# Kernel tuning notes

Measured on AMD Instinct MI355X. Metric: run time of the kernel, lower is better.

The kernel has to match this reference:

```python
import jax, jax.numpy as jnp
import numpy as np

B, S, DIN, D = 16, 1024, 64, 64

def setup_inputs() -> dict:
    key = jax.random.key(0)
    kx, kq, kk, kv, kaK, kaV = jax.random.split(key, 6)
    w_scale = 1.0 / np.sqrt(DIN)
    x = jax.random.normal(kx, (B, S, DIN), dtype=jnp.float32)
    Wq = jax.random.normal(kq, (DIN, D), dtype=jnp.float32) * w_scale
    Wk = jax.random.normal(kk, (DIN, D), dtype=jnp.float32) * w_scale
    Wv = jax.random.normal(kv, (DIN, D), dtype=jnp.float32) * w_scale
    # relative-position bias tables alpha_K/alpha_V: [S, S, D]
    alpha_K = jax.random.normal(kaK, (S, S, D), dtype=jnp.float32) * 0.02
    alpha_V = jax.random.normal(kaV, (S, S, D), dtype=jnp.float32) * 0.02
    return {"x": x, "Wq": Wq, "Wk": Wk, "Wv": Wv,
            "alpha_K": alpha_K, "alpha_V": alpha_V}

def reference(x, Wq, Wk, Wv, alpha_K, alpha_V):
    # Relation-aware self-attention (Shaw et al. style), vectorized form of
    # the original per-query loop:
    #   score[b,i,j] = q[b,i] . (k[b,j] + alpha_K[i,j]) / sqrt(D)
    #   z[b,i]       = sum_j softmax_j(score)[b,i,j] * (v[b,j] + alpha_V[i,j])
    d = Wq.shape[1]
    inv_sqrt_d = 1.0 / np.sqrt(d)
    q = jnp.einsum('bsf,fd->bsd', x, Wq)
    k = jnp.einsum('bsf,fd->bsd', x, Wk)
    v = jnp.einsum('bsf,fd->bsd', x, Wv)
    scores = (jnp.einsum('bid,bjd->bij', q, k)
              + jnp.einsum('bid,ijd->bij', q, alpha_K)) * inv_sqrt_d
    attn = jax.nn.softmax(scores, axis=-1)  # [B, S, S]
    z = (jnp.einsum('bij,bjd->bid', attn, v)
         + jnp.einsum('bij,ijd->bid', attn, alpha_V))
    return z, attn
```

## Files before the change

kernel.cpp:

```cpp
#include <hip/hip_runtime.h>
#include <hip/hip_fp16.h>
#include <hip/hip_bf16.h>


typedef unsigned short u16;
typedef __attribute__((ext_vector_type(8))) short bhalf8;
typedef __attribute__((ext_vector_type(4))) float fx4;

__device__ __forceinline__ short b16(float f) {
  __hip_bfloat16 h = __float2bfloat16(f);
  return *reinterpret_cast<short*>(&h);
}

__device__ __forceinline__ bhalf8 pack8(float4 a, float4 b) {
  bhalf8 r;
  r[0] = b16(a.x); r[1] = b16(a.y); r[2] = b16(a.z); r[3] = b16(a.w);
  r[4] = b16(b.x); r[5] = b16(b.y); r[6] = b16(b.z); r[7] = b16(b.w);
  return r;
}

__global__ __launch_bounds__(256) void k_proj(
    const float* __restrict__ x, const float* __restrict__ Wq,
    const float* __restrict__ Wk, const float* __restrict__ Wv,
    u16* __restrict__ qbf, u16* __restrict__ kbf, float* __restrict__ vf)
{
  __shared__ float wl[3 * 4096];
  const int t = threadIdx.x;
  for (int c = t; c < 4096; c += 256) {
    wl[c] = Wq[c]; wl[4096 + c] = Wk[c]; wl[8192 + c] = Wv[c];
  }
  __syncthreads();
  const int row = blockIdx.x * 64 + (t >> 2);
  const int dbase = (t & 3) * 16;
  float xr[64];
  const float4* xp = (const float4*)(x + (size_t)row * 64);
#pragma unroll
  for (int c = 0; c < 16; ++c) {
    float4 v = xp[c];
    xr[4*c] = v.x; xr[4*c+1] = v.y; xr[4*c+2] = v.z; xr[4*c+3] = v.w;
  }
  float aq[16], ak[16], av[16];
#pragma unroll
  for (int m = 0; m < 16; ++m) { aq[m] = 0.f; ak[m] = 0.f; av[m] = 0.f; }
#pragma unroll
  for (int f = 0; f < 64; ++f) {
    const float xv = xr[f];
    const float* wq = wl + f * 64 + dbase;
#pragma unroll
    for (int m = 0; m < 16; ++m) {
      aq[m] = fmaf(xv, wq[m], aq[m]);
      ak[m] = fmaf(xv, wq[4096 + m], ak[m]);
      av[m] = fmaf(xv, wq[8192 + m], av[m]);
    }
  }
  union { u16 u[16]; uint4 q[2]; } pq, pk;
#pragma unroll
  for (int m = 0; m < 16; ++m) { pq.u[m] = (u16)b16(aq[m]); pk.u[m] = (u16)b16(ak[m]); }
  const size_t o = (size_t)row * 64 + dbase;
  *(uint4*)(qbf + o) = pq.q[0]; *(uint4*)(qbf + o + 8) = pq.q[1];
  *(uint4*)(kbf + o) = pk.q[0]; *(uint4*)(kbf + o + 8) = pk.q[1];
  float4* vo = (float4*)(vf + o);
  vo[0] = make_float4(av[0], av[1], av[2], av[3]);
  vo[1] = make_float4(av[4], av[5], av[6], av[7]);
  vo[2] = make_float4(av[8], av[9], av[10], av[11]);
  vo[3] = make_float4(av[12], av[13], av[14], av[15]);
}

__global__ __launch_bounds__(256) void k_qk(
    const u16* __restrict__ qbf, const u16* __restrict__ kbf, __half* __restrict__ qkw)
{
  const int t = threadIdx.x, l = t & 63, w = t >> 6;
  const int b = blockIdx.x & 15, it = blockIdx.x >> 4;
  const int lr = l & 15, lg = l >> 4;
  const int i0 = it * 64 + w * 16;
  const u16* qp = qbf + (size_t)(b * 1024 + i0 + lr) * 64 + lg * 8;
  bhalf8 a0 = *(const bhalf8*)(qp);
  bhalf8 a1 = *(const bhalf8*)(qp + 32);
  for (int jt = 0; jt < 64; ++jt) {
    const int j0 = jt * 16;
    const u16* kp = kbf + (size_t)(b * 1024 + j0 + lr) * 64 + lg * 8;
    bhalf8 b0 = *(const bhalf8*)(kp);
    bhalf8 b1 = *(const bhalf8*)(kp + 32);
    fx4 acc = {0.f, 0.f, 0.f, 0.f};
    acc = __builtin_amdgcn_mfma_f32_16x16x32_bf16(a0, b0, acc, 0, 0, 0);
    acc = __builtin_amdgcn_mfma_f32_16x16x32_bf16(a1, b1, acc, 0, 0, 0);
#pragma unroll
    for (int r = 0; r < 4; ++r) {
      const int i = i0 + lg * 4 + r;
      qkw[((size_t)i * 16 + b) * 1024 + j0 + lr] = __float2half(acc[r]);
    }
  }
}

#define SLD2 516
__global__ __launch_bounds__(256, 4) void k_core(
    const float* __restrict__ aK, const float* __restrict__ aV,
    const u16* __restrict__ qbf, const __half* __restrict__ qkw,
    float* __restrict__ attn_out, float* __restrict__ za)
{
  __shared__ float sl[16 * SLD2];
  __shared__ float stats[64];
  const int i = blockIdx.x;
  const int t = threadIdx.x, l = t & 63, w = t >> 6;
  const int lr = l & 15, lg = l >> 4;

  const u16* qp = qbf + (size_t)(lr * 1024 + i) * 64 + lg * 8;
  bhalf8 a0 = *(const bhalf8*)(qp);
  bhalf8 a1 = *(const bhalf8*)(qp + 32);

  float zc[16];
#pragma unroll
  for (int b = 0; b < 16; ++b) zc[b] = 0.f;

  for (int h = 0; h < 2; ++h) {
    const __half* qk = qkw + (size_t)i * 16384 + h * 512;
    for (int c = t; c < 1024; c += 256) {
      const int b = c >> 6;
      const int j8 = (c & 63) * 8;
      const __half2* hp = (const __half2*)(qk + (size_t)b * 1024 + j8);
      float2 f0 = __half22float2(hp[0]);
      float2 f1 = __half22float2(hp[1]);
      float2 f2 = __half22float2(hp[2]);
      float2 f3 = __half22float2(hp[3]);
      float* dst = sl + b * SLD2 + j8;
      *(float4*)(dst)     = make_float4(f0.x, f0.y, f1.x, f1.y);
      *(float4*)(dst + 4) = make_float4(f2.x, f2.y, f3.x, f3.y);
    }
    __syncthreads();

    for (int tt = 0; tt < 8; ++tt) {
      const int j0 = (w + tt * 4) * 16;
      const float* ap = aK + ((size_t)i * 1024 + h * 512 + j0 + lr) * 64 + lg * 8;
      float4 c0 = *(const float4*)(ap);
      float4 c1 = *(const float4*)(ap + 4);
      float4 c2 = *(const float4*)(ap + 32);
      float4 c3 = *(const float4*)(ap + 36);
      fx4 acc = {0.f, 0.f, 0.f, 0.f};
      acc = __builtin_amdgcn_mfma_f32_16x16x32_bf16(a0, pack8(c0, c1), acc, 0, 0, 0);
      acc = __builtin_amdgcn_mfma_f32_16x16x32_bf16(a1, pack8(c2, c3), acc, 0, 0, 0);
#pragma unroll
      for (int r = 0; r < 4; ++r)
        sl[(lg * 4 + r) * SLD2 + j0 + lr] += acc[r];
    }
    __syncthreads();

    if (h == 0) {
#pragma unroll
      for (int rr = 0; rr < 4; ++rr) {
        const int row = w * 4 + rr;
        float* rp = sl + row * SLD2;
        float v8[8]; float mx = -3.0e30f;
#pragma unroll
        for (int c = 0; c < 8; ++c) { v8[c] = rp[c * 64 + l]; mx = fmaxf(mx, v8[c]); }
#pragma unroll
        for (int off = 32; off; off >>= 1) mx = fmaxf(mx, __shfl_xor(mx, off));
        float sum = 0.f;
        float* ao = attn_out + ((size_t)row * 1024 + i) * 1024;
#pragma unroll
        for (int c = 0; c < 8; ++c) {
          float e = __expf((v8[c] - mx) * 0.125f);
          sum += e; rp[c * 64 + l] = e;
          ao[c * 64 + l] = e;
        }
#pragma unroll
        for (int off = 32; off; off >>= 1) sum += __shfl_xor(sum, off);
        if (l == 0) { stats[row] = mx; stats[16 + row] = sum; }
      }
    } else {
#pragma unroll
      for (int rr = 0; rr < 4; ++rr) {
        const int row = w * 4 + rr;
        float* rp = sl + row * SLD2;
        float v8[8]; float mx = -3.0e30f;
#pragma unroll
        for (int c = 0; c < 8; ++c) { v8[c] = rp[c * 64 + l]; mx = fmaxf(mx, v8[c]); }
#pragma unroll
        for (int off = 32; off; off >>= 1) mx = fmaxf(mx, __shfl_xor(mx, off));
        const float m1 = stats[row];
        const float m  = fmaxf(m1, mx);
        const float corr = __expf((m1 - m) * 0.125f);
        float e8[8]; float sum = 0.f;
#pragma unroll
        for (int c = 0; c < 8; ++c) {
          e8[c] = __expf((v8[c] - m) * 0.125f);
          sum += e8[c]; rp[c * 64 + l] = e8[c];
        }
#pragma unroll
        for (int off = 32; off; off >>= 1) sum += __shfl_xor(sum, off);
        const float inv = 1.0f / (stats[16 + row] * corr + sum);
        float* ao = attn_out + ((size_t)row * 1024 + i) * 1024 + 512;
#pragma unroll
        for (int c = 0; c < 8; ++c) ao[c * 64 + l] = e8[c] * inv;
        if (l == 0) { stats[32 + row] = corr; stats[48 + row] = inv; }
      }
    }
    __syncthreads();

    if (h == 1) {
#pragma unroll
      for (int b = 0; b < 16; ++b) zc[b] *= stats[32 + b];
    }
    const float* avp = aV + ((size_t)i * 1024 + h * 512 + w * 128) * 64 + l;
    for (int jg = 0; jg < 32; ++jg) {
      const int jl = w * 128 + jg * 4;
      float a0v = avp[(size_t)(jg * 4 + 0) * 64];
      float a1v = avp[(size_t)(jg * 4 + 1) * 64];
      float a2v = avp[(size_t)(jg * 4 + 2) * 64];
      float a3v = avp[(size_t)(jg * 4 + 3) * 64];
#pragma unroll
      for (int b = 0; b < 16; ++b) {
        float4 e4 = *(const float4*)(sl + b * SLD2 + jl);
        zc[b] = fmaf(e4.x, a0v, zc[b]);
        zc[b] = fmaf(e4.y, a1v, zc[b]);
        zc[b] = fmaf(e4.z, a2v, zc[b]);
        zc[b] = fmaf(e4.w, a3v, zc[b]);
      }
    }
    __syncthreads();
  }

#pragma unroll
  for (int b = 0; b < 16; ++b) sl[(w * 16 + b) * 64 + l] = zc[b];
  __syncthreads();
  for (int o = t; o < 1024; o += 256) {
    const int b = o >> 6, d = o & 63;
    float s = sl[b * 64 + d] + sl[(16 + b) * 64 + d]
            + sl[(32 + b) * 64 + d] + sl[(48 + b) * 64 + d];
    za[((size_t)i * 16 + b) * 64 + d] = s * stats[48 + b];
  }

#pragma unroll
  for (int rr = 0; rr < 4; ++rr) {
    const int row = w * 4 + rr;
    const float f = stats[32 + row] * stats[48 + row];
    float* ao = attn_out + ((size_t)row * 1024 + i) * 1024;
#pragma unroll
    for (int c = 0; c < 8; ++c) ao[c * 64 + l] *= f;
  }
}

__global__ __launch_bounds__(256) void k_zv(
    const float* __restrict__ attn, const float* __restrict__ vf,
    const float* __restrict__ za, float* __restrict__ zout)
{
  __shared__ __align__(16) u16 vt[64 * 40];
  const int t = threadIdx.x, l = t & 63, w = t >> 6;
  const int b = blockIdx.x & 15, it = blockIdx.x >> 4;
  const int lr = l & 15, lg = l >> 4;
  const int iw = it * 64 + w * 16;
  fx4 acc[4];
#pragma unroll
  for (int n = 0; n < 4; ++n) acc[n] = (fx4){0.f, 0.f, 0.f, 0.f};
  const int jl = t >> 3;
  const int c0 = (t & 7) * 8;
  for (int ks = 0; ks < 32; ++ks) {
    const int j0 = ks * 32;
    const float* vp = vf + (size_t)(b * 1024 + j0 + jl) * 64 + c0;
    float4 v0 = *(const float4*)(vp);
    float4 v1 = *(const float4*)(vp + 4);
    __syncthreads();
    vt[(c0 + 0) * 40 + jl] = (u16)b16(v0.x);
    vt[(c0 + 1) * 40 + jl] = (u16)b16(v0.y);
    vt[(c0 + 2) * 40 + jl] = (u16)b16(v0.z);
    vt[(c0 + 3) * 40 + jl] = (u16)b16(v0.w);
    vt[(c0 + 4) * 40 + jl] = (u16)b16(v1.x);
    vt[(c0 + 5) * 40 + jl] = (u16)b16(v1.y);
    vt[(c0 + 6) * 40 + jl] = (u16)b16(v1.z);
    vt[(c0 + 7) * 40 + jl] = (u16)b16(v1.w);
    __syncthreads();
    const float* apr = attn + (size_t)(b * 1024 + iw + lr) * 1024 + j0 + lg * 8;
    float4 t0 = *(const float4*)(apr);
    float4 t1 = *(const float4*)(apr + 4);
    bhalf8 af = pack8(t0, t1);
#pragma unroll
    for (int n = 0; n < 4; ++n) {
      bhalf8 bf = *(const bhalf8*)(vt + (n * 16 + lr) * 40 + lg * 8);
      acc[n] = __builtin_amdgcn_mfma_f32_16x16x32_bf16(af, bf, acc[n], 0, 0, 0);
    }
  }
#pragma unroll
  for (int n = 0; n < 4; ++n) {
#pragma unroll
    for (int r = 0; r < 4; ++r) {
      const int i = iw + lg * 4 + r;
      const int dd = n * 16 + lr;
      zout[((size_t)b * 1024 + i) * 64 + dd] = acc[n][r] + za[((size_t)i * 16 + b) * 64 + dd];
    }
  }
}

extern "C" void kernel_launch(void* const* d_in, const int* in_sizes, int n_in,
                              void* d_out, int out_size, void* d_ws, size_t ws_size,
                              hipStream_t stream)
{
  const float* x  = (const float*)d_in[0];
  const float* Wq = (const float*)d_in[1];
  const float* Wk = (const float*)d_in[2];
  const float* Wv = (const float*)d_in[3];
  const float* aK = (const float*)d_in[4];
  const float* aV = (const float*)d_in[5];
  float* zout = (float*)d_out;
  float* attn_out = zout + (size_t)16 * 1024 * 64;

  char* ws = (char*)d_ws;
  u16*    qbf = (u16*)(ws);
  u16*    kbf = (u16*)(ws + (size_t)2  * 1024 * 1024);
  float*  vf  = (float*)(ws + (size_t)4  * 1024 * 1024);
  float*  za  = (float*)(ws + (size_t)8  * 1024 * 1024);
  __half* qkw = (__half*)(ws + (size_t)12 * 1024 * 1024);

  hipLaunchKernelGGL(k_proj, dim3(256),  dim3(256), 0, stream, x, Wq, Wk, Wv, qbf, kbf, vf);
  hipLaunchKernelGGL(k_qk,   dim3(256),  dim3(256), 0, stream, qbf, kbf, qkw);
  hipLaunchKernelGGL(k_core, dim3(1024), dim3(256), 0, stream, aK, aV, qbf, qkw, attn_out, za);
  hipLaunchKernelGGL(k_zv,   dim3(256),  dim3(256), 0, stream, attn_out, vf, za, zout);
}
```

Before: 230.0 us.

## Compute attn·alpha_V with bf16 MFMA via transposed LDS tile and vectorize softmax I/O

Replaces the scalar FMA loop that accumulated probabilities times alpha_V with bf16 MFMA 16x16x32 instructions. Probabilities are stored as bf16 in place in shared memory, and alpha_V is staged as a transposed bf16 tile in a new LDS buffer, with the next tile's global loads prefetched into registers. Softmax row loads and stores and the final attn rescale now use float4 accesses, and the qk fp16 loads become single 16-byte loads. The cost is bf16 rounding of the probabilities and alpha_V, plus two extra barriers for each 32-column step.

```diff
diff --git a/kernel.cpp b/kernel.cpp
--- a/kernel.cpp
+++ b/kernel.cpp
@@ -93,12 +93,14 @@
 }
 
 #define SLD2 516
+#define PADJ 40
 __global__ __launch_bounds__(256, 4) void k_core(
     const float* __restrict__ aK, const float* __restrict__ aV,
     const u16* __restrict__ qbf, const __half* __restrict__ qkw,
     float* __restrict__ attn_out, float* __restrict__ za)
 {
-  __shared__ float sl[16 * SLD2];
+  __shared__ __align__(16) float sl[16 * SLD2];
+  __shared__ __align__(16) u16 vt[64 * PADJ];
   __shared__ float stats[64];
   const int i = blockIdx.x;
   const int t = threadIdx.x, l = t & 63, w = t >> 6;
@@ -108,20 +110,22 @@
   bhalf8 a0 = *(const bhalf8*)(qp);
   bhalf8 a1 = *(const bhalf8*)(qp + 32);
 
-  float zc[16];
-#pragma unroll
-  for (int b = 0; b < 16; ++b) zc[b] = 0.f;
+  fx4 zacc = {0.f, 0.f, 0.f, 0.f};
+
+  const int jA = t >> 4;
+  const int dA = (t & 15) * 4;
 
   for (int h = 0; h < 2; ++h) {
     const __half* qk = qkw + (size_t)i * 16384 + h * 512;
     for (int c = t; c < 1024; c += 256) {
       const int b = c >> 6;
       const int j8 = (c & 63) * 8;
-      const __half2* hp = (const __half2*)(qk + (size_t)b * 1024 + j8);
-      float2 f0 = __half22float2(hp[0]);
-      float2 f1 = __half22float2(hp[1]);
-      float2 f2 = __half22float2(hp[2]);
-      float2 f3 = __half22float2(hp[3]);
+      uint4 u = *(const uint4*)(qk + (size_t)b * 1024 + j8);
+      const __half2* hh = (const __half2*)&u;
+      float2 f0 = __half22float2(hh[0]);
+      float2 f1 = __half22float2(hh[1]);
+      float2 f2 = __half22float2(hh[2]);
+      float2 f3 = __half22float2(hh[3]);
       float* dst = sl + b * SLD2 + j8;
       *(float4*)(dst)     = make_float4(f0.x, f0.y, f1.x, f1.y);
       *(float4*)(dst + 4) = make_float4(f2.x, f2.y, f3.x, f3.y);
@@ -149,19 +153,24 @@
       for (int rr = 0; rr < 4; ++rr) {
         const int row = w * 4 + rr;
         float* rp = sl + row * SLD2;
-        float v8[8]; float mx = -3.0e30f;
-#pragma unroll
-        for (int c = 0; c < 8; ++c) { v8[c] = rp[c * 64 + l]; mx = fmaxf(mx, v8[c]); }
+        float4 x0 = *(const float4*)(rp + l * 8);
+        float4 x1 = *(const float4*)(rp + l * 8 + 4);
+        float v8[8] = {x0.x, x0.y, x0.z, x0.w, x1.x, x1.y, x1.z, x1.w};
+        float mx = -3.0e30f;
+#pragma unroll
+        for (int c = 0; c < 8; ++c) mx = fmaxf(mx, v8[c]);
 #pragma unroll
         for (int off = 32; off; off >>= 1) mx = fmaxf(mx, __shfl_xor(mx, off));
-        float sum = 0.f;
+        float e8[8]; float sum = 0.f;
+#pragma unroll
+        for (int c = 0; c < 8; ++c) { e8[c] = __expf((v8[c] - mx) * 0.125f); sum += e8[c]; }
         float* ao = attn_out + ((size_t)row * 1024 + i) * 1024;
-#pragma unroll
-        for (int c = 0; c < 8; ++c) {
-          float e = __expf((v8[c] - mx) * 0.125f);
-          sum += e; rp[c * 64 + l] = e;
-          ao[c * 64 + l] = e;
-        }
+        *(float4*)(ao + l * 8)     = make_float4(e8[0], e8[1], e8[2], e8[3]);
+        *(float4*)(ao + l * 8 + 4) = make_float4(e8[4], e8[5], e8[6], e8[7]);
+        bhalf8 eb;
+#pragma unroll
+        for (int c = 0; c < 8; ++c) eb[c] = b16(e8[c]);
+        *(bhalf8*)((u16*)rp + l * 8) = eb;
 #pragma unroll
         for (int off = 32; off; off >>= 1) sum += __shfl_xor(sum, off);
         if (l == 0) { stats[row] = mx; stats[16 + row] = sum; }
@@ -171,9 +180,12 @@
       for (int rr = 0; rr < 4; ++rr) {
         const int row = w * 4 + rr;
         float* rp = sl + row * SLD2;
-        float v8[8]; float mx = -3.0e30f;
-#pragma unroll
-        for (int c = 0; c < 8; ++c) { v8[c] = rp[c * 64 + l]; mx = fmaxf(mx, v8[c]); }
+        float4 x0 = *(const float4*)(rp + l * 8);
+        float4 x1 = *(const float4*)(rp + l * 8 + 4);
+        float v8[8] = {x0.x, x0.y, x0.z, x0.w, x1.x, x1.y, x1.z, x1.w};
+        float mx = -3.0e30f;
+#pragma unroll
+        for (int c = 0; c < 8; ++c) mx = fmaxf(mx, v8[c]);
 #pragma unroll
         for (int off = 32; off; off >>= 1) mx = fmaxf(mx, __shfl_xor(mx, off));
         const float m1 = stats[row];
@@ -181,16 +193,17 @@
         const float corr = __expf((m1 - m) * 0.125f);
         float e8[8]; float sum = 0.f;
 #pragma unroll
-        for (int c = 0; c < 8; ++c) {
-          e8[c] = __expf((v8[c] - m) * 0.125f);
-          sum += e8[c]; rp[c * 64 + l] = e8[c];
-        }
+        for (int c = 0; c < 8; ++c) { e8[c] = __expf((v8[c] - m) * 0.125f); sum += e8[c]; }
+        bhalf8 eb;
+#pragma unroll
+        for (int c = 0; c < 8; ++c) eb[c] = b16(e8[c]);
+        *(bhalf8*)((u16*)rp + l * 8) = eb;
 #pragma unroll
         for (int off = 32; off; off >>= 1) sum += __shfl_xor(sum, off);
         const float inv = 1.0f / (stats[16 + row] * corr + sum);
         float* ao = attn_out + ((size_t)row * 1024 + i) * 1024 + 512;
-#pragma unroll
-        for (int c = 0; c < 8; ++c) ao[c * 64 + l] = e8[c] * inv;
+        *(float4*)(ao + l * 8)     = make_float4(e8[0]*inv, e8[1]*inv, e8[2]*inv, e8[3]*inv);
+        *(float4*)(ao + l * 8 + 4) = make_float4(e8[4]*inv, e8[5]*inv, e8[6]*inv, e8[7]*inv);
         if (l == 0) { stats[32 + row] = corr; stats[48 + row] = inv; }
       }
     }
@@ -198,35 +211,41 @@
 
     if (h == 1) {
 #pragma unroll
-      for (int b = 0; b < 16; ++b) zc[b] *= stats[32 + b];
-    }
-    const float* avp = aV + ((size_t)i * 1024 + h * 512 + w * 128) * 64 + l;
-    for (int jg = 0; jg < 32; ++jg) {
-      const int jl = w * 128 + jg * 4;
-      float a0v = avp[(size_t)(jg * 4 + 0) * 64];
-      float a1v = avp[(size_t)(jg * 4 + 1) * 64];
-      float a2v = avp[(size_t)(jg * 4 + 2) * 64];
-      float a3v = avp[(size_t)(jg * 4 + 3) * 64];
-#pragma unroll
-      for (int b = 0; b < 16; ++b) {
-        float4 e4 = *(const float4*)(sl + b * SLD2 + jl);
-        zc[b] = fmaf(e4.x, a0v, zc[b]);
-        zc[b] = fmaf(e4.y, a1v, zc[b]);
-        zc[b] = fmaf(e4.z, a2v, zc[b]);
-        zc[b] = fmaf(e4.w, a3v, zc[b]);
+      for (int r = 0; r < 4; ++r) zacc[r] *= stats[32 + lg * 4 + r];
+    }
+    float4 pa, pb;
+    {
+      const float* ap = aV + ((size_t)i * 1024 + h * 512 + jA) * 64 + dA;
+      pa = *(const float4*)(ap);
+      pb = *(const float4*)(ap + 1024);
+    }
+    for (int it = 0; it < 16; ++it) {
+      __syncthreads();
+      vt[(dA + 0) * PADJ + jA] = (u16)b16(pa.x);
+      vt[(dA + 1) * PADJ + jA] = (u16)b16(pa.y);
+      vt[(dA + 2) * PADJ + jA] = (u16)b16(pa.z);
+      vt[(dA + 3) * PADJ + jA] = (u16)b16(pa.w);
+      vt[(dA + 0) * PADJ + jA + 16] = (u16)b16(pb.x);
+      vt[(dA + 1) * PADJ + jA + 16] = (u16)b16(pb.y);
+      vt[(dA + 2) * PADJ + jA + 16] = (u16)b16(pb.z);
+      vt[(dA + 3) * PADJ + jA + 16] = (u16)b16(pb.w);
+      if (it < 15) {
+        const float* ap = aV + ((size_t)i * 1024 + h * 512 + (it + 1) * 32 + jA) * 64 + dA;
+        pa = *(const float4*)(ap);
+        pb = *(const float4*)(ap + 1024);
       }
-    }
-    __syncthreads();
-  }
-
-#pragma unroll
-  for (int b = 0; b < 16; ++b) sl[(w * 16 + b) * 64 + l] = zc[b];
-  __syncthreads();
-  for (int o = t; o < 1024; o += 256) {
-    const int b = o >> 6, d = o & 63;
-    float s = sl[b * 64 + d] + sl[(16 + b) * 64 + d]
-            + sl[(32 + b) * 64 + d] + sl[(48 + b) * 64 + d];
-    za[((size_t)i * 16 + b) * 64 + d] = s * stats[48 + b];
+      __syncthreads();
+      bhalf8 ea = *(const bhalf8*)((const u16*)(sl + (size_t)lr * SLD2) + it * 32 + lg * 8);
+      bhalf8 bv = *(const bhalf8*)(vt + (w * 16 + lr) * PADJ + lg * 8);
+      zacc = __builtin_amdgcn_mfma_f32_16x16x32_bf16(ea, bv, zacc, 0, 0, 0);
+    }
+    __syncthreads();
+  }
+
+#pragma unroll
+  for (int r = 0; r < 4; ++r) {
+    const int b = lg * 4 + r;
+    za[((size_t)i * 16 + b) * 64 + w * 16 + lr] = zacc[r] * stats[48 + b];
   }
 
 #pragma unroll
@@ -234,8 +253,10 @@
     const int row = w * 4 + rr;
     const float f = stats[32 + row] * stats[48 + row];
     float* ao = attn_out + ((size_t)row * 1024 + i) * 1024;
-#pragma unroll
-    for (int c = 0; c < 8; ++c) ao[c * 64 + l] *= f;
+    float4 u0 = *(const float4*)(ao + l * 8);
+    float4 u1 = *(const float4*)(ao + l * 8 + 4);
+    *(float4*)(ao + l * 8)     = make_float4(u0.x*f, u0.y*f, u0.z*f, u0.w*f);
+    *(float4*)(ao + l * 8 + 4) = make_float4(u1.x*f, u1.y*f, u1.z*f, u1.w*f);
   }
 }
 
```

Result: no change. 225.8 us (-1.8%).
